# Kernel optimization log

Hardware: AMD Instinct MI355X
Metric: run time of the kernel (lower is better)

## Reference

```python
import jax, jax.numpy as jnp
import numpy as np

N_NODES = 100000
N_EDGES = 6400000
IN_CH, HID, OUT_CH = 14, 16, 8


def setup_inputs() -> dict:
    key = jax.random.key(0)
    ks = jax.random.split(key, 10)
    x = jax.random.normal(ks[0], (N_NODES, IN_CH), dtype=jnp.float32)
    edge_index = jax.random.randint(ks[1], (2, N_EDGES), 0, N_NODES, dtype=jnp.int64)
    edge_attr = jax.random.normal(ks[2], (N_EDGES, 4), dtype=jnp.float32)
    # SAGEConv params: lin_l (neighbor aggr, with bias), lin_r (root, no bias)
    def glorot(k, shape):
        fan_in = shape[1]
        return jax.random.normal(k, shape, dtype=jnp.float32) / jnp.sqrt(jnp.float32(fan_in))
    W1_l = glorot(ks[3], (HID, IN_CH)); b1 = jnp.zeros((HID,), jnp.float32)
    W1_r = glorot(ks[4], (HID, IN_CH))
    W2_l = glorot(ks[5], (OUT_CH, HID)); b2 = jnp.zeros((OUT_CH,), jnp.float32)
    W2_r = glorot(ks[6], (OUT_CH, HID))
    return {"x": x, "edge_index": edge_index, "edge_attr": edge_attr,
            "W1_l": W1_l, "b1": b1, "W1_r": W1_r,
            "W2_l": W2_l, "b2": b2, "W2_r": W2_r}


def sage_conv(x, src, dst, W_l, b_l, W_r):
    # mean aggregation of neighbor features at destination nodes
    msg = x[src]                                            # [E, F]
    s = jax.ops.segment_sum(msg, dst, num_segments=N_NODES)  # [N, F]
    cnt = jax.ops.segment_sum(jnp.ones((src.shape[0],), x.dtype), dst,
                              num_segments=N_NODES)
    mean = s / jnp.maximum(cnt, 1.0)[:, None]
    # out = lin_l(mean) + lin_r(x)
    return mean @ W_l.T + b_l + x @ W_r.T


def reference(x, edge_index, edge_attr, W1_l, b1, W1_r, W2_l, b2, W2_r):
    src, dst = edge_index[0], edge_index[1]
    h = jax.nn.relu(sage_conv(x, src, dst, W1_l, b1, W1_r))
    # F.dropout(training=self.training) -> identity in eval mode
    out = sage_conv(h, src, dst, W2_l, b2, W2_r)
    return out
```

## Files before the change

### kernel.cpp

```cpp
#include <hip/hip_runtime.h>

#define N_NODES 100000
#define N_EDGES 6400000
#define IN_CH 14
#define HID 16
#define OUT_CH 8

#define NBINS 1024
#define BINW 98
#define HB 256
#define BF_THREADS 1024
#define BF_TILE 8192
#define BF_EPT (BF_TILE / BF_THREADS)
#define N_TILES ((N_EDGES + BF_TILE - 1) / BF_TILE)
#define SORT_CAP 7168
#define LHN 128

__device__ __forceinline__ unsigned short f2bf(float f) {
    unsigned u = __float_as_uint(f);
    u += 0x7fffu + ((u >> 16) & 1u);
    return (unsigned short)(u >> 16);
}

__global__ void cast_x_kernel(const float* __restrict__ x, unsigned short* __restrict__ xb) {
    int i = blockIdx.x * blockDim.x + threadIdx.x;
    if (i >= (NBINS * BINW) * 16) return;
    int n = i >> 4, c = i & 15;
    float v = (n < N_NODES && c < IN_CH) ? x[n * IN_CH + c] : 0.0f;
    xb[i] = f2bf(v);
}

__global__ void hist_kernel(const uint4* __restrict__ dst4, int* __restrict__ partial) {
    __shared__ int lh[NBINS];
    lh[threadIdx.x] = 0; lh[threadIdx.x + 256] = 0;
    lh[threadIdx.x + 512] = 0; lh[threadIdx.x + 768] = 0;
    __syncthreads();
    const int n4 = N_EDGES / 4;
    for (int i = blockIdx.x * blockDim.x + threadIdx.x; i < n4;
         i += gridDim.x * blockDim.x) {
        uint4 d = dst4[i];
        atomicAdd(&lh[d.x / BINW], 1);
        atomicAdd(&lh[d.y / BINW], 1);
        atomicAdd(&lh[d.z / BINW], 1);
        atomicAdd(&lh[d.w / BINW], 1);
    }
    __syncthreads();
    partial[blockIdx.x * NBINS + threadIdx.x]       = lh[threadIdx.x];
    partial[blockIdx.x * NBINS + threadIdx.x + 256] = lh[threadIdx.x + 256];
    partial[blockIdx.x * NBINS + threadIdx.x + 512] = lh[threadIdx.x + 512];
    partial[blockIdx.x * NBINS + threadIdx.x + 768] = lh[threadIdx.x + 768];
}

__global__ void scan_kernel(const int* __restrict__ partial,
                            int* __restrict__ binCount,
                            int* __restrict__ binbase, int* __restrict__ tail) {
    __shared__ int s[NBINS];
    int t = threadIdx.x;
    int v = 0;
    for (int g = 0; g < HB; ++g) v += partial[g * NBINS + t];
    binCount[t] = v;
    s[t] = v;
    __syncthreads();
    for (int d = 1; d < NBINS; d <<= 1) {
        int a = (t >= d) ? s[t - d] : 0;
        __syncthreads();
        s[t] += a;
        __syncthreads();
    }
    int excl = s[t] - v;
    binbase[t] = excl;
    tail[t] = excl;
}

__global__ __launch_bounds__(BF_THREADS)
void binfill_kernel(const uint4* __restrict__ src4, const uint4* __restrict__ dst4,
                    int* __restrict__ tail, unsigned* __restrict__ binbuf) {
    __shared__ unsigned stile[BF_TILE];
    __shared__ unsigned short stbin[BF_TILE];
    __shared__ int lh[NBINS];
    __shared__ int lx[NBINS];
    __shared__ int lbase[NBINS];

    const int t = threadIdx.x;
    const long long tb = (long long)blockIdx.x * BF_TILE;

    lh[t] = 0;
    __syncthreads();

    unsigned epack[BF_EPT];
    int      ebin[BF_EPT];
    int      erank[BF_EPT];

#pragma unroll
    for (int sw = 0; sw < BF_EPT / 4; ++sw) {
        long long u = tb / 4 + (long long)sw * BF_THREADS + t;
        int k = sw * 4;
        if (u * 4 < N_EDGES) {
            uint4 s = src4[u];
            uint4 d = dst4[u];
            unsigned b;
            b = d.x / BINW; epack[k+0] = s.x | ((d.x - b*BINW) << 17); ebin[k+0] = (int)b; erank[k+0] = atomicAdd(&lh[b], 1);
            b = d.y / BINW; epack[k+1] = s.y | ((d.y - b*BINW) << 17); ebin[k+1] = (int)b; erank[k+1] = atomicAdd(&lh[b], 1);
            b = d.z / BINW; epack[k+2] = s.z | ((d.z - b*BINW) << 17); ebin[k+2] = (int)b; erank[k+2] = atomicAdd(&lh[b], 1);
            b = d.w / BINW; epack[k+3] = s.w | ((d.w - b*BINW) << 17); ebin[k+3] = (int)b; erank[k+3] = atomicAdd(&lh[b], 1);
        } else {
            ebin[k+0] = ebin[k+1] = ebin[k+2] = ebin[k+3] = -1;
        }
    }
    __syncthreads();

    int v = lh[t];
    lx[t] = v;
    __syncthreads();
    for (int d = 1; d < NBINS; d <<= 1) {
        int a = (t >= d) ? lx[t - d] : 0;
        __syncthreads();
        lx[t] += a;
        __syncthreads();
    }
    int excl = lx[t] - v;
    lbase[t] = atomicAdd(&tail[t], v);
    __syncthreads();
    lx[t] = excl;
    __syncthreads();

#pragma unroll
    for (int k = 0; k < BF_EPT; ++k) {
        if (ebin[k] >= 0) {
            int pos = lx[ebin[k]] + erank[k];
            stile[pos] = epack[k];
            stbin[pos] = (unsigned short)ebin[k];
        }
    }
    __syncthreads();

    int cnt = (int)((N_EDGES - tb < BF_TILE) ? (N_EDGES - tb) : BF_TILE);
    for (int i = t; i < cnt; i += BF_THREADS) {
        int b = stbin[i];
        unsigned idx = (unsigned)(lbase[b] + (i - lx[b]));
        if (idx < (unsigned)N_EDGES) binbuf[idx] = stile[i];
    }
}

__global__ __launch_bounds__(512)
void sortagg1_kernel(const unsigned* __restrict__ xb, const float* __restrict__ x,
                     unsigned* __restrict__ binbuf,
                     const int* __restrict__ binbase, const int* __restrict__ binCount,
                     int* __restrict__ rowptr, int* __restrict__ deg,
                     const float* __restrict__ W_l, const float* __restrict__ bias,
                     const float* __restrict__ W_r,
                     float* __restrict__ h_f32, unsigned short* __restrict__ h_bf16) {
    __shared__ unsigned sbuf[SORT_CAP];
    __shared__ int lhist[LHN];
    __shared__ int lsc[LHN];
    __shared__ int loff[LHN];
    __shared__ int lcur[LHN];

    const int b = blockIdx.x;
    const int t = threadIdx.x;

    int beg = binbase[b];
    int cnt = binCount[b];
    if (beg < 0) beg = 0;
    if (cnt < 0) cnt = 0;
    if (cnt > SORT_CAP) cnt = SORT_CAP;
    if (beg + cnt > N_EDGES) cnt = N_EDGES - beg;

    if (t < LHN) lhist[t] = 0;
    __syncthreads();

    for (int i = t; i < cnt; i += 512)
        atomicAdd(&lhist[binbuf[beg + i] >> 17], 1);
    __syncthreads();

    int v = (t < LHN) ? lhist[t] : 0;
    if (t < LHN) lsc[t] = v;
    __syncthreads();
    for (int d = 1; d < LHN; d <<= 1) {
        int a = (t >= d && t < LHN) ? lsc[t - d] : 0;
        __syncthreads();
        if (t < LHN) lsc[t] += a;
        __syncthreads();
    }
    if (t < LHN) {
        int excl = lsc[t] - v;
        loff[t] = excl;
        lcur[t] = excl;
        if (t < BINW) {
            int gn = b * BINW + t;
            if (gn < N_NODES) { rowptr[gn] = beg + excl; deg[gn] = v; }
        }
    }
    __syncthreads();

    for (int i = t; i < cnt; i += 512) {
        unsigned w = binbuf[beg + i];
        unsigned ld = w >> 17;
        int pos = atomicAdd(&lcur[ld], 1);
        if (pos < cnt) sbuf[pos] = w & 0x1FFFFu;
    }
    __syncthreads();

    for (int i = t; i < cnt; i += 512)
        binbuf[beg + i] = sbuf[i];

    const int g = t >> 3;
    const int l = t & 7;
    float m0[2], m1[2];
#pragma unroll
    for (int p = 0; p < 2; ++p) {
        m0[p] = 0.0f; m1[p] = 0.0f;
        int n = g + 64 * p;
        if (n < BINW) {
            int dg = lhist[n];
            int off = loff[n];
            float a0 = 0.0f, a1 = 0.0f;
            int i = 0;
            for (; i + 4 <= dg; i += 4) {
                unsigned s0 = sbuf[off + i], s1 = sbuf[off + i + 1];
                unsigned s2 = sbuf[off + i + 2], s3 = sbuf[off + i + 3];
                unsigned u0 = xb[s0 * 8 + l];
                unsigned u1 = xb[s1 * 8 + l];
                unsigned u2 = xb[s2 * 8 + l];
                unsigned u3 = xb[s3 * 8 + l];
                a0 += __uint_as_float(u0 << 16);  a1 += __uint_as_float(u0 & 0xffff0000u);
                a0 += __uint_as_float(u1 << 16);  a1 += __uint_as_float(u1 & 0xffff0000u);
                a0 += __uint_as_float(u2 << 16);  a1 += __uint_as_float(u2 & 0xffff0000u);
                a0 += __uint_as_float(u3 << 16);  a1 += __uint_as_float(u3 & 0xffff0000u);
            }
            for (; i < dg; ++i) {
                unsigned u0 = xb[sbuf[off + i] * 8 + l];
                a0 += __uint_as_float(u0 << 16);  a1 += __uint_as_float(u0 & 0xffff0000u);
            }
            float inv = 1.0f / fmaxf((float)dg, 1.0f);
            m0[p] = a0 * inv; m1[p] = a1 * inv;
        }
    }
    __syncthreads();

    float* smean = (float*)sbuf;
#pragma unroll
    for (int p = 0; p < 2; ++p) {
        int n = g + 64 * p;
        if (n < BINW) {
            smean[n * 16 + 2 * l]     = m0[p];
            smean[n * 16 + 2 * l + 1] = m1[p];
        }
    }
    __syncthreads();

    const int nodeBase = b * BINW;
    for (int i = t; i < BINW * HID; i += 512) {
        int n = i >> 4, oc = i & 15;
        int gn = nodeBase + n;
        if (gn >= N_NODES) break;
        float a = bias[oc];
#pragma unroll
        for (int k = 0; k < IN_CH; ++k)
            a = fmaf(smean[n * 16 + k], W_l[oc * IN_CH + k],
                     fmaf(x[gn * IN_CH + k], W_r[oc * IN_CH + k], a));
        float vv = fmaxf(a, 0.0f);
        h_f32[gn * HID + oc] = vv;
        h_bf16[gn * HID + oc] = f2bf(vv);
    }
}

__global__ __launch_bounds__(256)
void agg2_kernel(const unsigned* __restrict__ hb,
                 const float* __restrict__ h_f32,
                 const unsigned* __restrict__ csr,
                 const int* __restrict__ rowptr, const int* __restrict__ deg,
                 const float* __restrict__ W_l, const float* __restrict__ bias,
                 const float* __restrict__ W_r, float* __restrict__ out) {
    __shared__ float smean[4][8][16];

    const int t = threadIdx.x;
    const int wv = t >> 6;
    const int lane = t & 63;
    const int g = lane >> 3;
    const int l = lane & 7;
    const int node = (blockIdx.x * 4 + wv) * 8 + g;

    int beg = rowptr[node];
    int d = deg[node];
    if (beg < 0) beg = 0;
    if (d < 0) d = 0;
    if (beg + d > N_EDGES) d = N_EDGES - beg;

    float a0 = 0.0f, a1 = 0.0f;
    int i = 0;
    for (; i + 8 <= d; i += 8) {
        unsigned s0 = csr[beg + i]     & 0x1FFFFu;
        unsigned s1 = csr[beg + i + 1] & 0x1FFFFu;
        unsigned s2 = csr[beg + i + 2] & 0x1FFFFu;
        unsigned s3 = csr[beg + i + 3] & 0x1FFFFu;
        unsigned s4 = csr[beg + i + 4] & 0x1FFFFu;
        unsigned s5 = csr[beg + i + 5] & 0x1FFFFu;
        unsigned s6 = csr[beg + i + 6] & 0x1FFFFu;
        unsigned s7 = csr[beg + i + 7] & 0x1FFFFu;
        unsigned u0 = hb[s0 * 8 + l];
        unsigned u1 = hb[s1 * 8 + l];
        unsigned u2 = hb[s2 * 8 + l];
        unsigned u3 = hb[s3 * 8 + l];
        unsigned u4 = hb[s4 * 8 + l];
        unsigned u5 = hb[s5 * 8 + l];
        unsigned u6 = hb[s6 * 8 + l];
        unsigned u7 = hb[s7 * 8 + l];
        a0 += __uint_as_float(u0 << 16);        a1 += __uint_as_float(u0 & 0xffff0000u);
        a0 += __uint_as_float(u1 << 16);        a1 += __uint_as_float(u1 & 0xffff0000u);
        a0 += __uint_as_float(u2 << 16);        a1 += __uint_as_float(u2 & 0xffff0000u);
        a0 += __uint_as_float(u3 << 16);        a1 += __uint_as_float(u3 & 0xffff0000u);
        a0 += __uint_as_float(u4 << 16);        a1 += __uint_as_float(u4 & 0xffff0000u);
        a0 += __uint_as_float(u5 << 16);        a1 += __uint_as_float(u5 & 0xffff0000u);
        a0 += __uint_as_float(u6 << 16);        a1 += __uint_as_float(u6 & 0xffff0000u);
        a0 += __uint_as_float(u7 << 16);        a1 += __uint_as_float(u7 & 0xffff0000u);
    }
    for (; i < d; ++i) {
        unsigned s0 = csr[beg + i] & 0x1FFFFu;
        unsigned u0 = hb[s0 * 8 + l];
        a0 += __uint_as_float(u0 << 16);        a1 += __uint_as_float(u0 & 0xffff0000u);
    }
    float inv = 1.0f / fmaxf((float)d, 1.0f);
    smean[wv][g][2 * l]     = a0 * inv;
    smean[wv][g][2 * l + 1] = a1 * inv;

    {
        int n8 = lane >> 3;
        int oc = lane & 7;
        int gn = (blockIdx.x * 4 + wv) * 8 + n8;
        float a = bias[oc];
#pragma unroll
        for (int k = 0; k < HID; ++k)
            a = fmaf(smean[wv][n8][k], W_l[oc * HID + k],
                     fmaf(h_f32[gn * HID + k], W_r[oc * HID + k], a));
        out[gn * OUT_CH + oc] = a;
    }
}

extern "C" void kernel_launch(void* const* d_in, const int* in_sizes, int n_in,
                              void* d_out, int out_size, void* d_ws, size_t ws_size,
                              hipStream_t stream) {
    const float* x    = (const float*)d_in[0];
    const int* eidx   = (const int*)d_in[1];
    const float* W1_l = (const float*)d_in[3];
    const float* b1   = (const float*)d_in[4];
    const float* W1_r = (const float*)d_in[5];
    const float* W2_l = (const float*)d_in[6];
    const float* b2   = (const float*)d_in[7];
    const float* W2_r = (const float*)d_in[8];
    float* out = (float*)d_out;

    const uint4* src4 = (const uint4*)eidx;
    const uint4* dst4 = (const uint4*)(eidx + N_EDGES);

    int*            wsi      = (int*)d_ws;
    unsigned*       binbuf   = (unsigned*)wsi;
    int*            partial  = wsi + 6400000;
    int*            binCount = wsi + 6662144;
    int*            binbase  = wsi + 6663168;
    int*            tail     = wsi + 6664192;
    unsigned short* x_bf16   = (unsigned short*)(wsi + 6665216);
    unsigned short* h_bf16   = (unsigned short*)(wsi + 7468032);
    float*          h_f32    = (float*)(wsi + 8268032);
    int*            rowptr   = wsi + 9868032;
    int*            deg      = wsi + 9968384;

    cast_x_kernel<<<(NBINS * BINW * 16 + 1023) / 1024, 1024, 0, stream>>>(x, x_bf16);
    hist_kernel<<<HB, 256, 0, stream>>>(dst4, partial);
    scan_kernel<<<1, NBINS, 0, stream>>>(partial, binCount, binbase, tail);
    binfill_kernel<<<N_TILES, BF_THREADS, 0, stream>>>(src4, dst4, tail, binbuf);
    sortagg1_kernel<<<NBINS, 512, 0, stream>>>((const unsigned*)x_bf16, x, binbuf,
                                               binbase, binCount, rowptr, deg,
                                               W1_l, b1, W1_r, h_f32, h_bf16);
    agg2_kernel<<<3125, 256, 0, stream>>>((const unsigned*)h_bf16, h_f32, binbuf,
                                          rowptr, deg, W2_l, b2, W2_r, out);
}
```

Measured before the change: 327.5 us.

## Replace global histogram pass with fixed-capacity per-bin slabs and wave-shuffle scans

```diff
diff --git a/kernel.cpp b/kernel.cpp
--- a/kernel.cpp
+++ b/kernel.cpp
@@ -8,12 +8,12 @@
 
 #define NBINS 1024
 #define BINW 98
-#define HB 256
+#define SLAB 7168
+#define BINBUF_WORDS (NBINS * SLAB)
 #define BF_THREADS 1024
 #define BF_TILE 8192
 #define BF_EPT (BF_TILE / BF_THREADS)
 #define N_TILES ((N_EDGES + BF_TILE - 1) / BF_TILE)
-#define SORT_CAP 7168
 #define LHN 128
 
 __device__ __forceinline__ unsigned short f2bf(float f) {
@@ -22,54 +22,14 @@
     return (unsigned short)(u >> 16);
 }
 
-__global__ void cast_x_kernel(const float* __restrict__ x, unsigned short* __restrict__ xb) {
+__global__ void prep_kernel(const float* __restrict__ x, unsigned short* __restrict__ xb,
+                            int* __restrict__ tail) {
     int i = blockIdx.x * blockDim.x + threadIdx.x;
+    if (i < NBINS) tail[i] = 0;
     if (i >= (NBINS * BINW) * 16) return;
     int n = i >> 4, c = i & 15;
     float v = (n < N_NODES && c < IN_CH) ? x[n * IN_CH + c] : 0.0f;
     xb[i] = f2bf(v);
-}
-
-__global__ void hist_kernel(const uint4* __restrict__ dst4, int* __restrict__ partial) {
-    __shared__ int lh[NBINS];
-    lh[threadIdx.x] = 0; lh[threadIdx.x + 256] = 0;
-    lh[threadIdx.x + 512] = 0; lh[threadIdx.x + 768] = 0;
-    __syncthreads();
-    const int n4 = N_EDGES / 4;
-    for (int i = blockIdx.x * blockDim.x + threadIdx.x; i < n4;
-         i += gridDim.x * blockDim.x) {
-        uint4 d = dst4[i];
-        atomicAdd(&lh[d.x / BINW], 1);
-        atomicAdd(&lh[d.y / BINW], 1);
-        atomicAdd(&lh[d.z / BINW], 1);
-        atomicAdd(&lh[d.w / BINW], 1);
-    }
-    __syncthreads();
-    partial[blockIdx.x * NBINS + threadIdx.x]       = lh[threadIdx.x];
-    partial[blockIdx.x * NBINS + threadIdx.x + 256] = lh[threadIdx.x + 256];
-    partial[blockIdx.x * NBINS + threadIdx.x + 512] = lh[threadIdx.x + 512];
-    partial[blockIdx.x * NBINS + threadIdx.x + 768] = lh[threadIdx.x + 768];
-}
-
-__global__ void scan_kernel(const int* __restrict__ partial,
-                            int* __restrict__ binCount,
-                            int* __restrict__ binbase, int* __restrict__ tail) {
-    __shared__ int s[NBINS];
-    int t = threadIdx.x;
-    int v = 0;
-    for (int g = 0; g < HB; ++g) v += partial[g * NBINS + t];
-    binCount[t] = v;
-    s[t] = v;
-    __syncthreads();
-    for (int d = 1; d < NBINS; d <<= 1) {
-        int a = (t >= d) ? s[t - d] : 0;
-        __syncthreads();
-        s[t] += a;
-        __syncthreads();
-    }
-    int excl = s[t] - v;
-    binbase[t] = excl;
-    tail[t] = excl;
 }
 
 __global__ __launch_bounds__(BF_THREADS)
@@ -79,9 +39,12 @@
     __shared__ unsigned short stbin[BF_TILE];
     __shared__ int lh[NBINS];
     __shared__ int lx[NBINS];
-    __shared__ int lbase[NBINS];
+    __shared__ int lofs[NBINS];
+    __shared__ int wsum[16];
 
     const int t = threadIdx.x;
+    const int lane = t & 63;
+    const int wv = t >> 6;
     const long long tb = (long long)blockIdx.x * BF_TILE;
 
     lh[t] = 0;
@@ -110,18 +73,27 @@
     __syncthreads();
 
     int v = lh[t];
-    lx[t] = v;
-    __syncthreads();
-    for (int d = 1; d < NBINS; d <<= 1) {
-        int a = (t >= d) ? lx[t - d] : 0;
-        __syncthreads();
-        lx[t] += a;
-        __syncthreads();
-    }
-    int excl = lx[t] - v;
-    lbase[t] = atomicAdd(&tail[t], v);
-    __syncthreads();
-    lx[t] = excl;
+    int incl = v;
+#pragma unroll
+    for (int d = 1; d < 64; d <<= 1) {
+        int o = __shfl_up(incl, d, 64);
+        if (lane >= d) incl += o;
+    }
+    if (lane == 63) wsum[wv] = incl;
+    __syncthreads();
+    if (t < 16) {
+        int s = wsum[t];
+        int si = s;
+#pragma unroll
+        for (int d = 1; d < 16; d <<= 1) {
+            int o = __shfl_up(si, d, 16);
+            if (t >= d) si += o;
+        }
+        wsum[t] = si - s;
+    }
+    __syncthreads();
+    lx[t] = incl - v + wsum[wv];
+    lofs[t] = atomicAdd(&tail[t], v);
     __syncthreads();
 
 #pragma unroll
@@ -137,34 +109,32 @@
     int cnt = (int)((N_EDGES - tb < BF_TILE) ? (N_EDGES - tb) : BF_TILE);
     for (int i = t; i < cnt; i += BF_THREADS) {
         int b = stbin[i];
-        unsigned idx = (unsigned)(lbase[b] + (i - lx[b]));
-        if (idx < (unsigned)N_EDGES) binbuf[idx] = stile[i];
+        int slot = lofs[b] + (i - lx[b]);
+        if ((unsigned)slot < (unsigned)SLAB)
+            binbuf[b * SLAB + slot] = stile[i];
     }
 }
 
 __global__ __launch_bounds__(512)
 void sortagg1_kernel(const unsigned* __restrict__ xb, const float* __restrict__ x,
-                     unsigned* __restrict__ binbuf,
-                     const int* __restrict__ binbase, const int* __restrict__ binCount,
+                     unsigned* __restrict__ binbuf, const int* __restrict__ tail,
                      int* __restrict__ rowptr, int* __restrict__ deg,
                      const float* __restrict__ W_l, const float* __restrict__ bias,
                      const float* __restrict__ W_r,
                      float* __restrict__ h_f32, unsigned short* __restrict__ h_bf16) {
-    __shared__ unsigned sbuf[SORT_CAP];
+    __shared__ unsigned sbuf[SLAB];
     __shared__ int lhist[LHN];
-    __shared__ int lsc[LHN];
     __shared__ int loff[LHN];
     __shared__ int lcur[LHN];
+    __shared__ int wtot[2];
 
     const int b = blockIdx.x;
     const int t = threadIdx.x;
 
-    int beg = binbase[b];
-    int cnt = binCount[b];
-    if (beg < 0) beg = 0;
+    const int beg = b * SLAB;
+    int cnt = tail[b];
     if (cnt < 0) cnt = 0;
-    if (cnt > SORT_CAP) cnt = SORT_CAP;
-    if (beg + cnt > N_EDGES) cnt = N_EDGES - beg;
+    if (cnt > SLAB) cnt = SLAB;
 
     if (t < LHN) lhist[t] = 0;
     __syncthreads();
@@ -174,16 +144,16 @@
     __syncthreads();
 
     int v = (t < LHN) ? lhist[t] : 0;
-    if (t < LHN) lsc[t] = v;
-    __syncthreads();
-    for (int d = 1; d < LHN; d <<= 1) {
-        int a = (t >= d && t < LHN) ? lsc[t - d] : 0;
-        __syncthreads();
-        if (t < LHN) lsc[t] += a;
-        __syncthreads();
-    }
+    int incl = v;
+#pragma unroll
+    for (int d = 1; d < 64; d <<= 1) {
+        int o = __shfl_up(incl, d, 64);
+        if ((t & 63) >= d) incl += o;
+    }
+    if (t < LHN && (t & 63) == 63) wtot[t >> 6] = incl;
+    __syncthreads();
     if (t < LHN) {
-        int excl = lsc[t] - v;
+        int excl = incl - v + ((t >= 64) ? wtot[0] : 0);
         loff[t] = excl;
         lcur[t] = excl;
         if (t < BINW) {
@@ -285,7 +255,7 @@
     int d = deg[node];
     if (beg < 0) beg = 0;
     if (d < 0) d = 0;
-    if (beg + d > N_EDGES) d = N_EDGES - beg;
+    if (beg + d > BINBUF_WORDS) d = BINBUF_WORDS - beg;
 
     float a0 = 0.0f, a1 = 0.0f;
     int i = 0;
@@ -355,23 +325,17 @@
 
     int*            wsi      = (int*)d_ws;
     unsigned*       binbuf   = (unsigned*)wsi;
-    int*            partial  = wsi + 6400000;
-    int*            binCount = wsi + 6662144;
-    int*            binbase  = wsi + 6663168;
-    int*            tail     = wsi + 6664192;
-    unsigned short* x_bf16   = (unsigned short*)(wsi + 6665216);
-    unsigned short* h_bf16   = (unsigned short*)(wsi + 7468032);
-    float*          h_f32    = (float*)(wsi + 8268032);
-    int*            rowptr   = wsi + 9868032;
-    int*            deg      = wsi + 9968384;
-
-    cast_x_kernel<<<(NBINS * BINW * 16 + 1023) / 1024, 1024, 0, stream>>>(x, x_bf16);
-    hist_kernel<<<HB, 256, 0, stream>>>(dst4, partial);
-    scan_kernel<<<1, NBINS, 0, stream>>>(partial, binCount, binbase, tail);
+    int*            tail     = wsi + 7340032;
+    unsigned short* x_bf16   = (unsigned short*)(wsi + 7341056);
+    unsigned short* h_bf16   = (unsigned short*)(wsi + 8143872);
+    float*          h_f32    = (float*)(wsi + 8943872);
+    int*            rowptr   = wsi + 10543872;
+    int*            deg      = wsi + 10644224;
+
+    prep_kernel<<<(NBINS * BINW * 16 + 1023) / 1024, 1024, 0, stream>>>(x, x_bf16, tail);
     binfill_kernel<<<N_TILES, BF_THREADS, 0, stream>>>(src4, dst4, tail, binbuf);
-    sortagg1_kernel<<<NBINS, 512, 0, stream>>>((const unsigned*)x_bf16, x, binbuf,
-                                               binbase, binCount, rowptr, deg,
-                                               W1_l, b1, W1_r, h_f32, h_bf16);
+    sortagg1_kernel<<<NBINS, 512, 0, stream>>>((const unsigned*)x_bf16, x, binbuf, tail,
+                                               rowptr, deg, W1_l, b1, W1_r, h_f32, h_bf16);
     agg2_kernel<<<3125, 256, 0, stream>>>((const unsigned*)h_bf16, h_f32, binbuf,
                                           rowptr, deg, W2_l, b2, W2_r, out);
 }
```

Result: faster. 301.2 us (-8.0%).
